# Optimization experiments

Hardware: AMD Instinct MI355X
Metric: run time of the kernel (lower is better)

## Reference

```python
import jax, jax.numpy as jnp
import numpy as np

HALF_LOG_2PI = 0.9189385332046727  # 0.5*log(2*pi)


def _sum_layer(prod, logits):
    # prod: [B, R, KK] child log-probs; logits: [R, KK, K] unnormalized sum weights
    W = jax.nn.softmax(logits, axis=1)            # normalized mixture weights
    m = jnp.max(prod, axis=-1, keepdims=True)     # stable logsumexp via einsum
    e = jnp.exp(prod - m)                         # [B, R, KK]
    s = jnp.einsum('brc,rck->brk', e, W)          # [B, R, K]
    return jnp.log(s) + m


def setup_inputs() -> dict:
    key = jax.random.key(0)
    ks = jax.random.split(key, 12)
    B, F, K = 8192, 256, 8
    inp = {
        'x': jax.random.normal(ks[0], (B, F), dtype=jnp.float32),
        'mu': jax.random.normal(ks[1], (F, K), dtype=jnp.float32),
        'log_sigma': jax.random.uniform(ks[2], (F, K), dtype=jnp.float32),
    }
    R = F // 2
    for i in range(8):
        inp['w%d' % i] = jax.random.normal(ks[3 + i], (R, K * K, K), dtype=jnp.float32)
        R //= 2
    inp['root_w'] = jax.random.normal(ks[11], (K,), dtype=jnp.float32)
    return inp


def reference(x, mu, log_sigma, w0, w1, w2, w3, w4, w5, w6, w7, root_w):
    # Gaussian leaf log-probs: [B, F, K]
    z = (x[:, :, None] - mu) * jnp.exp(-log_sigma)
    h = -0.5 * z * z - log_sigma - HALF_LOG_2PI
    # Alternating product (pair adjacent regions) / sum (mix KK -> K) layers
    for w in (w0, w1, w2, w3, w4, w5, w6, w7):
        B, R, K = h.shape
        prod = (h[:, 0::2, :, None] + h[:, 1::2, None, :]).reshape(B, R // 2, K * K)
        h = _sum_layer(prod, w)
    # Root sum node over the K dists of the single remaining region -> [B]
    lp = h[:, 0, :] + jax.nn.log_softmax(root_w)
    return jax.scipy.special.logsumexp(lp, axis=-1)
```

## Files before the change

kernel.cpp:

```cpp
#include <hip/hip_runtime.h>
#include <math.h>

#define NTH 256

static constexpr float HLP = 0.9189385332046727f;

typedef __attribute__((ext_vector_type(2))) _Float16 half2v;
typedef __attribute__((ext_vector_type(2))) __fp16   fp16x2;

static constexpr int WTTd = 61440;
static constexpr int AOF2 = 65280;
static constexpr int BOF2 = 67328;
static constexpr int ROF2 = 69376;
static constexpr int L1NF = 69632;
static constexpr int L1MF = L1NF + 2097152;
static constexpr int L3NF = L1MF + 524288;
static constexpr int L3MF = L3NF + 524288;
static constexpr size_t WS_NEED_B = (size_t)(L3MF + 131072) * 4;

__device__ __forceinline__ half2v pkrtz(float a, float b) {
  return __builtin_bit_cast(half2v, __builtin_amdgcn_cvt_pkrtz(a, b));
}
__device__ __forceinline__ half2v u2h(unsigned u) {
  return __builtin_bit_cast(half2v, u);
}
__device__ __forceinline__ unsigned h2u(half2v h) {
  return __builtin_bit_cast(unsigned, h);
}
__device__ __forceinline__ float dd(half2v a, half2v b, float c) {
#if __has_builtin(__builtin_amdgcn_fdot2)
  return __builtin_amdgcn_fdot2(__builtin_bit_cast(fp16x2, a),
                                __builtin_bit_cast(fp16x2, b), c, false);
#else
  return fmaf((float)a[0], (float)b[0], fmaf((float)a[1], (float)b[1], c));
#endif
}
__device__ __forceinline__ float max8(const float* s) {
  float m = s[0];
  #pragma unroll
  for (int k = 1; k < 8; ++k) m = fmaxf(m, s[k]);
  return m;
}

__device__ __forceinline__ void leaf_ii(float xv, const float* mu8, const float* A8,
                                        const float* B8, half2v* ii, float* M) {
  float h[8];
  float m = -3.0e38f;
  #pragma unroll
  for (int k = 0; k < 8; ++k) {
    const float z = (xv - mu8[k]) * A8[k];
    h[k] = fmaf(-0.5f * z, z, B8[k]);
    m = fmaxf(m, h[k]);
  }
  #pragma unroll
  for (int k = 0; k < 8; ++k) {
    const float n = __expf(h[k] - m);
    ii[k] = pkrtz(n, n);
  }
  *M = m;
}
__device__ __forceinline__ void leaf_pk(float xv, const float* mu8, const float* A8,
                                        const float* B8, half2v* pk, float* M) {
  float h[8];
  float m = -3.0e38f;
  #pragma unroll
  for (int k = 0; k < 8; ++k) {
    const float z = (xv - mu8[k]) * A8[k];
    h[k] = fmaf(-0.5f * z, z, B8[k]);
    m = fmaxf(m, h[k]);
  }
  #pragma unroll
  for (int p = 0; p < 4; ++p) {
    const float n0 = __expf(h[2 * p] - m);
    const float n1 = __expf(h[2 * p + 1] - m);
    pk[p] = pkrtz(n0, n1);
  }
  *M = m;
}

template<int G, bool OUT_II>
__device__ __forceinline__ void combine_d2(const uint4* __restrict__ WL,
                                           const half2v (&na)[G][8],
                                           const half2v (&nb)[G][4],
                                           half2v (&oii)[G][8],
                                           half2v (&opk)[G][4],
                                           float (&M)[G]) {
  float s[G][8];
  #pragma unroll
  for (int g = 0; g < G; ++g)
    #pragma unroll
    for (int k = 0; k < 8; ++k) s[g][k] = 0.f;

  #pragma unroll
  for (int i = 0; i < 8; ++i) {
    half2v e[G][4];
    #pragma unroll
    for (int g = 0; g < G; ++g) {
      e[g][0] = na[g][i] * nb[g][0];
      e[g][1] = na[g][i] * nb[g][1];
      e[g][2] = na[g][i] * nb[g][2];
      e[g][3] = na[g][i] * nb[g][3];
    }
    #pragma unroll
    for (int k = 0; k < 8; ++k) {
      const uint4 w = WL[i * 8 + k];
      #pragma unroll
      for (int g = 0; g < G; ++g) {
        float acc = s[g][k];
        acc = dd(e[g][0], u2h(w.x), acc);
        acc = dd(e[g][1], u2h(w.y), acc);
        acc = dd(e[g][2], u2h(w.z), acc);
        acc = dd(e[g][3], u2h(w.w), acc);
        s[g][k] = acc;
      }
    }
  }
  #pragma unroll
  for (int g = 0; g < G; ++g) {
    const float smax = max8(s[g]);
    const float inv = 1.0f / smax;
    if constexpr (OUT_II) {
      #pragma unroll
      for (int p = 0; p < 8; ++p) {
        const float n = s[g][p] * inv;
        oii[g][p] = pkrtz(n, n);
      }
    } else {
      #pragma unroll
      for (int p = 0; p < 4; ++p)
        opk[g][p] = pkrtz(s[g][2 * p] * inv, s[g][2 * p + 1] * inv);
    }
    M[g] += __logf(smax);
  }
}

__global__ __launch_bounds__(256) void spn_prep4(
    const float* __restrict__ ls,
    const float* __restrict__ w0, const float* __restrict__ w1,
    const float* __restrict__ w2, const float* __restrict__ w3,
    const float* __restrict__ w4, const float* __restrict__ w5,
    const float* __restrict__ w6, const float* __restrict__ w7,
    const float* __restrict__ root_w,
    float* __restrict__ ws)
{
  const int job = blockIdx.x * blockDim.x + threadIdx.x;
  unsigned* wdw = reinterpret_cast<unsigned*>(ws);
  if (job < 1920) {
    const int ridx = job >> 3, k = job & 7;
    const float* src;
    if (ridx < 128)      src = w0 + ridx * 512 + k;
    else if (ridx < 192) src = w1 + (ridx - 128) * 512 + k;
    else if (ridx < 224) src = w2 + (ridx - 192) * 512 + k;
    else                 src = w3 + (ridx - 224) * 512 + k;
    float v[64];
    float m = -3.0e38f;
    #pragma unroll
    for (int c = 0; c < 64; ++c) { v[c] = src[c * 8]; m = fmaxf(m, v[c]); }
    float t = 0.f;
    #pragma unroll
    for (int c = 0; c < 64; ++c) { v[c] = __expf(v[c] - m); t += v[c]; }
    const float inv = 1.0f / t;
    #pragma unroll
    for (int i = 0; i < 8; ++i)
      #pragma unroll
      for (int jp = 0; jp < 4; ++jp)
        wdw[ridx * 256 + (i * 8 + k) * 4 + jp] =
            h2u(pkrtz(v[i * 8 + 2 * jp] * inv, v[i * 8 + 2 * jp + 1] * inv));
  } else if (job < 2040) {
    const int j = job - 1920;
    const int reg = j >> 3, k = j & 7;
    const float* src;
    if (reg < 8)       src = w4 + reg * 512 + k;
    else if (reg < 12) src = w5 + (reg - 8) * 512 + k;
    else if (reg < 14) src = w6 + (reg - 12) * 512 + k;
    else               src = w7 + k;
    float v[64];
    float m = -3.0e38f;
    #pragma unroll
    for (int c = 0; c < 64; ++c) { v[c] = src[c * 8]; m = fmaxf(m, v[c]); }
    float t = 0.f;
    #pragma unroll
    for (int c = 0; c < 64; ++c) { v[c] = __expf(v[c] - m); t += v[c]; }
    const float inv = 1.0f / t;
    #pragma unroll
    for (int i = 0; i < 8; ++i)
      #pragma unroll
      for (int jp = 0; jp < 4; ++jp)
        wdw[WTTd + reg * 256 + k * 32 + (((i ^ k) & 7) << 2) + jp] =
            h2u(pkrtz(v[i * 8 + 2 * jp] * inv, v[i * 8 + 2 * jp + 1] * inv));
  } else if (job < 2040 + 2048) {
    const int i = job - 2040;
    const float l = ls[i];
    ws[AOF2 + i] = __expf(-l);
    ws[BOF2 + i] = -l - HLP;
  } else if (job == 2040 + 2048) {
    float m = -3.0e38f;
    for (int k = 0; k < 8; ++k) m = fmaxf(m, root_w[k]);
    float e[8]; float t = 0.f;
    for (int k = 0; k < 8; ++k) { e[k] = __expf(root_w[k] - m); t += e[k]; }
    const float inv = 1.0f / t;
    for (int k = 0; k < 8; ++k) ws[ROF2 + k] = e[k] * inv;
  }
}

__global__ __launch_bounds__(NTH, 4) void spn_L01d(
    const float* __restrict__ x,
    const float* __restrict__ mu,
    float* __restrict__ ws)
{
  __shared__ uint4 wsh4[192];
  __shared__ float lsh[96];
  const int tid = threadIdx.x;
  const int r1 = blockIdx.x >> 4;
  const int chunk = blockIdx.x & 15;
  const uint4* wg = reinterpret_cast<const uint4*>(ws);

  if (tid < 192) {
    const int reg = tid >> 6;
    const int rbase = (reg < 2) ? (2 * r1 + reg) : (128 + r1);
    wsh4[tid] = wg[rbase * 64 + (tid & 63)];
  }
  if (tid < 96) {
    const int f8 = r1 * 32;
    lsh[tid] = (tid < 32) ? mu[f8 + tid]
             : (tid < 64) ? ws[AOF2 + f8 + (tid - 32)]
                          : ws[BOF2 + f8 + (tid - 64)];
  }
  __syncthreads();

  const int b0 = chunk * 512 + tid;
  const float4 xv0 = *reinterpret_cast<const float4*>(x + (size_t)b0 * 256 + 4 * r1);
  const float4 xv1 = *reinterpret_cast<const float4*>(x + (size_t)(b0 + 256) * 256 + 4 * r1);

  half2v ii[2][8], pk[2][4];
  half2v cAii[2][8], cBpk[2][4];
  half2v dmy_ii[2][8], dmy_pk[2][4];
  float MA[2], MB[2];
  float Ma, Mb;

  leaf_ii(xv0.x, lsh + 0, lsh + 32, lsh + 64, ii[0], &Ma);
  leaf_pk(xv0.y, lsh + 8, lsh + 40, lsh + 72, pk[0], &Mb);
  MA[0] = Ma + Mb;
  leaf_ii(xv1.x, lsh + 0, lsh + 32, lsh + 64, ii[1], &Ma);
  leaf_pk(xv1.y, lsh + 8, lsh + 40, lsh + 72, pk[1], &Mb);
  MA[1] = Ma + Mb;
  combine_d2<2, true>(wsh4, ii, pk, cAii, dmy_pk, MA);

  leaf_ii(xv0.z, lsh + 16, lsh + 48, lsh + 80, ii[0], &Ma);
  leaf_pk(xv0.w, lsh + 24, lsh + 56, lsh + 88, pk[0], &Mb);
  MB[0] = Ma + Mb;
  leaf_ii(xv1.z, lsh + 16, lsh + 48, lsh + 80, ii[1], &Ma);
  leaf_pk(xv1.w, lsh + 24, lsh + 56, lsh + 88, pk[1], &Mb);
  MB[1] = Ma + Mb;
  combine_d2<2, false>(wsh4 + 64, ii, pk, dmy_ii, cBpk, MB);

  float M[2] = {MA[0] + MB[0], MA[1] + MB[1]};
  half2v n[2][4];
  combine_d2<2, false>(wsh4 + 128, cAii, cBpk, dmy_ii, n, M);

  uint4* outn = reinterpret_cast<uint4*>(ws + L1NF);
  outn[r1 * 8192 + b0]       = uint4{h2u(n[0][0]), h2u(n[0][1]), h2u(n[0][2]), h2u(n[0][3])};
  outn[r1 * 8192 + b0 + 256] = uint4{h2u(n[1][0]), h2u(n[1][1]), h2u(n[1][2]), h2u(n[1][3])};
  ws[L1MF + r1 * 8192 + b0]       = M[0];
  ws[L1MF + r1 * 8192 + b0 + 256] = M[1];
}

__device__ __forceinline__ void mk_ii(uint4 p, half2v* ii) {
  const half2v a0 = u2h(p.x), a1 = u2h(p.y), a2 = u2h(p.z), a3 = u2h(p.w);
  ii[0] = __builtin_shufflevector(a0, a0, 0, 0);
  ii[1] = __builtin_shufflevector(a0, a0, 1, 1);
  ii[2] = __builtin_shufflevector(a1, a1, 0, 0);
  ii[3] = __builtin_shufflevector(a1, a1, 1, 1);
  ii[4] = __builtin_shufflevector(a2, a2, 0, 0);
  ii[5] = __builtin_shufflevector(a2, a2, 1, 1);
  ii[6] = __builtin_shufflevector(a3, a3, 0, 0);
  ii[7] = __builtin_shufflevector(a3, a3, 1, 1);
}

__global__ __launch_bounds__(NTH, 4) void spn_L23d(float* __restrict__ ws)
{
  __shared__ uint4 wsh4[192];
  const int tid = threadIdx.x;
  const int r3 = blockIdx.x >> 5;
  const int chunk = blockIdx.x & 31;
  const uint4* wg = reinterpret_cast<const uint4*>(ws);

  if (tid < 192) {
    const int reg = tid >> 6;
    const int rbase = (reg < 2) ? (192 + 2 * r3 + reg) : (224 + r3);
    wsh4[tid] = wg[rbase * 64 + (tid & 63)];
  }
  __syncthreads();

  const int b = chunk * 256 + tid;
  const uint4* n4 = reinterpret_cast<const uint4*>(ws + L1NF);
  const uint4 p0 = n4[(4 * r3 + 0) * 8192 + b];
  const uint4 p1 = n4[(4 * r3 + 1) * 8192 + b];
  const uint4 p2 = n4[(4 * r3 + 2) * 8192 + b];
  const uint4 p3 = n4[(4 * r3 + 3) * 8192 + b];
  const float M0 = ws[L1MF + (4 * r3 + 0) * 8192 + b];
  const float M1 = ws[L1MF + (4 * r3 + 1) * 8192 + b];
  const float M2 = ws[L1MF + (4 * r3 + 2) * 8192 + b];
  const float M3 = ws[L1MF + (4 * r3 + 3) * 8192 + b];

  half2v ii[1][8], pk[1][4];
  half2v cAii[1][8], cBpk[1][4];
  half2v dmy_ii[1][8], dmy_pk[1][4];

  mk_ii(p0, ii[0]);
  pk[0][0] = u2h(p1.x); pk[0][1] = u2h(p1.y); pk[0][2] = u2h(p1.z); pk[0][3] = u2h(p1.w);
  float MA[1] = {M0 + M1};
  combine_d2<1, true>(wsh4, ii, pk, cAii, dmy_pk, MA);

  mk_ii(p2, ii[0]);
  pk[0][0] = u2h(p3.x); pk[0][1] = u2h(p3.y); pk[0][2] = u2h(p3.z); pk[0][3] = u2h(p3.w);
  float MB[1] = {M2 + M3};
  combine_d2<1, false>(wsh4 + 64, ii, pk, dmy_ii, cBpk, MB);

  float M[1] = {MA[0] + MB[0]};
  half2v n[1][4];
  combine_d2<1, false>(wsh4 + 128, cAii, cBpk, dmy_ii, n, M);

  reinterpret_cast<uint4*>(ws + L3NF)[r3 * 8192 + b] =
      uint4{h2u(n[0][0]), h2u(n[0][1]), h2u(n[0][2]), h2u(n[0][3])};
  ws[L3MF + r3 * 8192 + b] = M[0];
}

__device__ __forceinline__ float macTd(const uint4* __restrict__ Wr, int myk,
                                       const float* na, const half2v* nbpk) {
  float s = 0.f;
  #pragma unroll
  for (int i = 0; i < 8; ++i) {
    const uint4 w = Wr[myk * 8 + ((i ^ myk) & 7)];
    float T = dd(nbpk[0], u2h(w.x), 0.f);
    T = dd(nbpk[1], u2h(w.y), T);
    T = dd(nbpk[2], u2h(w.z), T);
    T = dd(nbpk[3], u2h(w.w), T);
    s = fmaf(na[i], T, s);
  }
  return s;
}

__global__ __launch_bounds__(NTH) void spn_taild(float* __restrict__ ws,
                                                 float* __restrict__ out)
{
  __shared__ uint4 wsh4[960];
  __shared__ float ssh[8];
  const int tid = threadIdx.x;
  const uint4* wg = reinterpret_cast<const uint4*>(ws);
  #pragma unroll
  for (int i = 0; i < 4; ++i) {
    const int idx = tid + i * 256;
    if (idx < 960) wsh4[idx] = wg[WTTd / 4 + idx];
  }
  if (tid < 8) ssh[tid] = ws[ROF2 + tid];
  __syncthreads();

  const int lane = tid & 63, wid = tid >> 6;
  const int myk = lane & 7, bsub = lane >> 3, gbase = lane & 56;
  const int b = blockIdx.x * 32 + wid * 8 + bsub;

  const uint4* n4 = reinterpret_cast<const uint4*>(ws + L3NF);

  float n4v[8], M4[8];
  #pragma unroll
  for (int r = 0; r < 8; ++r) {
    const uint4 pa = n4[(2 * r + 0) * 8192 + b];
    const uint4 pb = n4[(2 * r + 1) * 8192 + b];
    const float Ma = ws[L3MF + (2 * r + 0) * 8192 + b];
    const float Mb = ws[L3MF + (2 * r + 1) * 8192 + b];
    float na[8];
    const half2v a0 = u2h(pa.x), a1 = u2h(pa.y), a2 = u2h(pa.z), a3 = u2h(pa.w);
    na[0] = (float)a0[0]; na[1] = (float)a0[1];
    na[2] = (float)a1[0]; na[3] = (float)a1[1];
    na[4] = (float)a2[0]; na[5] = (float)a2[1];
    na[6] = (float)a3[0]; na[7] = (float)a3[1];
    half2v nbpk[4] = {u2h(pb.x), u2h(pb.y), u2h(pb.z), u2h(pb.w)};
    float s = macTd(wsh4 + r * 64, myk, na, nbpk);
    float m = s;
    m = fmaxf(m, __shfl_xor(m, 1)); m = fmaxf(m, __shfl_xor(m, 2)); m = fmaxf(m, __shfl_xor(m, 4));
    n4v[r] = s / m;
    M4[r] = Ma + Mb + __logf(m);
  }

  float n5v[4], M5[4];
  #pragma unroll
  for (int r = 0; r < 4; ++r) {
    float na[8]; half2v nbpk[4];
    #pragma unroll
    for (int i = 0; i < 8; ++i) na[i] = __shfl(n4v[2 * r], gbase + i, 64);
    #pragma unroll
    for (int p = 0; p < 4; ++p)
      nbpk[p] = pkrtz(__shfl(n4v[2 * r + 1], gbase + 2 * p, 64),
                      __shfl(n4v[2 * r + 1], gbase + 2 * p + 1, 64));
    float s = macTd(wsh4 + (8 + r) * 64, myk, na, nbpk);
    float m = s;
    m = fmaxf(m, __shfl_xor(m, 1)); m = fmaxf(m, __shfl_xor(m, 2)); m = fmaxf(m, __shfl_xor(m, 4));
    n5v[r] = s / m;
    M5[r] = M4[2 * r] + M4[2 * r + 1] + __logf(m);
  }

  float n6v[2], M6[2];
  #pragma unroll
  for (int r = 0; r < 2; ++r) {
    float na[8]; half2v nbpk[4];
    #pragma unroll
    for (int i = 0; i < 8; ++i) na[i] = __shfl(n5v[2 * r], gbase + i, 64);
    #pragma unroll
    for (int p = 0; p < 4; ++p)
      nbpk[p] = pkrtz(__shfl(n5v[2 * r + 1], gbase + 2 * p, 64),
                      __shfl(n5v[2 * r + 1], gbase + 2 * p + 1, 64));
    float s = macTd(wsh4 + (12 + r) * 64, myk, na, nbpk);
    float m = s;
    m = fmaxf(m, __shfl_xor(m, 1)); m = fmaxf(m, __shfl_xor(m, 2)); m = fmaxf(m, __shfl_xor(m, 4));
    n6v[r] = s / m;
    M6[r] = M5[2 * r] + M5[2 * r + 1] + __logf(m);
  }

  {
    float na[8]; half2v nbpk[4];
    #pragma unroll
    for (int i = 0; i < 8; ++i) na[i] = __shfl(n6v[0], gbase + i, 64);
    #pragma unroll
    for (int p = 0; p < 4; ++p)
      nbpk[p] = pkrtz(__shfl(n6v[1], gbase + 2 * p, 64),
                      __shfl(n6v[1], gbase + 2 * p + 1, 64));
    float s = macTd(wsh4 + 14 * 64, myk, na, nbpk);
    float m = s;
    m = fmaxf(m, __shfl_xor(m, 1)); m = fmaxf(m, __shfl_xor(m, 2)); m = fmaxf(m, __shfl_xor(m, 4));
    const float n7 = s / m;
    const float M7 = M6[0] + M6[1] + __logf(m);
    float prod = n7 * ssh[myk];
    prod += __shfl_xor(prod, 1); prod += __shfl_xor(prod, 2); prod += __shfl_xor(prod, 4);
    if (myk == 0) out[b] = M7 + __logf(prod);
  }
}

static constexpr int NW   = 130560;
static constexpr int AOFF = NW;
static constexpr int BOFF = NW + 2048;
static constexpr int ROFF = NW + 4096;

__device__ __forceinline__ void leaf_eval(float xv, const float* mu8, const float* A8,
                                          const float* B8, float* n, float* M) {
  float h[8];
  float m = -3.0e38f;
  #pragma unroll
  for (int k = 0; k < 8; ++k) {
    const float z = (xv - mu8[k]) * A8[k];
    h[k] = fmaf(-0.5f * z, z, B8[k]);
    m = fmaxf(m, h[k]);
  }
  #pragma unroll
  for (int k = 0; k < 8; ++k) n[k] = __expf(h[k] - m);
  *M = m;
}

__global__ __launch_bounds__(256) void spn_prep(
    const float* __restrict__ ls,
    const float* __restrict__ w0, const float* __restrict__ w1,
    const float* __restrict__ w2, const float* __restrict__ w3,
    const float* __restrict__ w4, const float* __restrict__ w5,
    const float* __restrict__ w6, const float* __restrict__ w7,
    const float* __restrict__ root_w,
    float* __restrict__ ws)
{
  const int job = blockIdx.x * blockDim.x + threadIdx.x;
  if (job < 2040) {
    const float* wl[8] = {w0, w1, w2, w3, w4, w5, w6, w7};
    int j = job, l = 0, base = 0, R = 128;
    while (j >= R * 8) { j -= R * 8; base += R * 512; R >>= 1; ++l; }
    const int r = j >> 3, k = j & 7;
    const float* src = wl[l] + r * 512 + k;
    float v[64];
    float m = -3.0e38f;
    #pragma unroll
    for (int c = 0; c < 64; ++c) { v[c] = src[c * 8]; m = fmaxf(m, v[c]); }
    float ssum = 0.f;
    #pragma unroll
    for (int c = 0; c < 64; ++c) { v[c] = __expf(v[c] - m); ssum += v[c]; }
    const float inv = 1.0f / ssum;
    float* dst = ws + base + r * 512 + k;
    #pragma unroll
    for (int c = 0; c < 64; ++c) dst[c * 8] = v[c] * inv;
  } else if (job < 2040 + 2048) {
    const int i = job - 2040;
    const float l = ls[i];
    ws[AOFF + i] = __expf(-l);
    ws[BOFF + i] = -l - HLP;
  } else if (job == 2040 + 2048) {
    float m = -3.0e38f;
    for (int k = 0; k < 8; ++k) m = fmaxf(m, root_w[k]);
    float e[8]; float ssum = 0.f;
    for (int k = 0; k < 8; ++k) { e[k] = __expf(root_w[k] - m); ssum += e[k]; }
    const float inv = 1.0f / ssum;
    for (int k = 0; k < 8; ++k) ws[ROFF + k] = e[k] * inv;
  }
}

__device__ __forceinline__ void mac64(const float* __restrict__ Wr,
                                      const float* na, const float* nb,
                                      float* s) {
  #pragma unroll
  for (int k = 0; k < 8; ++k) s[k] = 0.f;
  #pragma unroll
  for (int i = 0; i < 8; ++i) {
    const float ai = na[i];
    #pragma unroll
    for (int j = 0; j < 8; ++j) {
      const float e = ai * nb[j];
      const float4 wA = *reinterpret_cast<const float4*>(Wr + (i * 8 + j) * 8);
      const float4 wB = *reinterpret_cast<const float4*>(Wr + (i * 8 + j) * 8 + 4);
      s[0] = fmaf(e, wA.x, s[0]); s[1] = fmaf(e, wA.y, s[1]);
      s[2] = fmaf(e, wA.z, s[2]); s[3] = fmaf(e, wA.w, s[3]);
      s[4] = fmaf(e, wB.x, s[4]); s[5] = fmaf(e, wB.y, s[5]);
      s[6] = fmaf(e, wB.z, s[6]); s[7] = fmaf(e, wB.w, s[7]);
    }
  }
}

#define TB 8
static constexpr int PLA = 128 * 9 + 5;
static constexpr int PLB = 64 * 9 + 5;
static constexpr int NAO = 0;
static constexpr int NBO = TB * PLA;
static constexpr int MAO = NBO + TB * PLB;
static constexpr int MBO = MAO + TB * 128;
static constexpr int SMEM_F = MBO + TB * 64;

__global__ __launch_bounds__(NTH, 2) void spn_main_fb(
    const float* __restrict__ x,
    const float* __restrict__ mu,
    const float* __restrict__ ws,
    float* __restrict__ out)
{
  const float* leafA = ws + AOFF;
  const float* leafB = ws + BOFF;
  const float* srw   = ws + ROFF;

  __shared__ float smem[SMEM_F];

  const int tid = threadIdx.x;
  const int bB = blockIdx.x * TB;

  {
    const float* W0 = ws;
    for (int it = tid; it < TB * 128; it += NTH) {
      const int bb = it & (TB - 1), r = it >> 3;
      float na[8], nb[8], Ma, Mb;
      const int f0 = 2 * r;
      const float xv0 = x[(bB + bb) * 256 + f0];
      const float xv1 = x[(bB + bb) * 256 + f0 + 1];
      leaf_eval(xv0, mu + f0 * 8, leafA + f0 * 8, leafB + f0 * 8, na, &Ma);
      leaf_eval(xv1, mu + f0 * 8 + 8, leafA + f0 * 8 + 8, leafB + f0 * 8 + 8, nb, &Mb);
      float s[8];
      mac64(W0 + r * 512, na, nb, s);
      const float smax = max8(s);
      const float inv = 1.0f / smax;
      const int ob = NAO + bb * PLA + r * 9;
      #pragma unroll
      for (int k = 0; k < 8; ++k) smem[ob + k] = s[k] * inv;
      smem[MAO + bb * 128 + r] = Ma + Mb + __logf(smax);
    }
  }
  __syncthreads();

  int pinO = NAO, poutO = NBO;
  int MinO = MAO, MoutO = MBO;
  int PLIN = PLA, PLOUT = PLB;
  int Rin = 128;
  const float* Wl = ws + 128 * 512;
  for (int l = 1; l < 7; ++l) {
    const int Rout = Rin >> 1;
    for (int it = tid; it < TB * Rout; it += NTH) {
      const int bb = it & (TB - 1), r = it >> 3;
      float na[8], nb[8];
      const int ia = pinO + bb * PLIN + (2 * r) * 9;
      #pragma unroll
      for (int i = 0; i < 8; ++i) { na[i] = smem[ia + i]; nb[i] = smem[ia + 9 + i]; }
      float s[8];
      mac64(Wl + r * 512, na, nb, s);
      const float smax = max8(s);
      const float inv = 1.0f / smax;
      const int ob = poutO + bb * PLOUT + r * 9;
      #pragma unroll
      for (int k = 0; k < 8; ++k) smem[ob + k] = s[k] * inv;
      smem[MoutO + bb * Rout + r] =
          smem[MinO + bb * Rin + 2 * r] + smem[MinO + bb * Rin + 2 * r + 1] + __logf(smax);
    }
    __syncthreads();
    int t;
    t = pinO; pinO = poutO; poutO = t;
    t = MinO; MinO = MoutO; MoutO = t;
    t = PLIN; PLIN = PLOUT; PLOUT = t;
    Rin = Rout;
    Wl += Rout * 512;
  }

  for (int it = tid; it < TB; it += NTH) {
    const int bb = it;
    float na[8], nb[8];
    const int ia = pinO + bb * PLIN;
    #pragma unroll
    for (int i = 0; i < 8; ++i) { na[i] = smem[ia + i]; nb[i] = smem[ia + 9 + i]; }
    float s[8];
    mac64(Wl, na, nb, s);
    float acc = 0.f;
    #pragma unroll
    for (int k = 0; k < 8; ++k) acc = fmaf(s[k], srw[k], acc);
    out[bB + bb] = smem[MinO + bb * 2] + smem[MinO + bb * 2 + 1] + __logf(acc);
  }
}

extern "C" void kernel_launch(void* const* d_in, const int* in_sizes, int n_in,
                              void* d_out, int out_size, void* d_ws, size_t ws_size,
                              hipStream_t stream) {
  (void)in_sizes; (void)n_in; (void)out_size;
  const float* x      = (const float*)d_in[0];
  const float* mu     = (const float*)d_in[1];
  const float* ls     = (const float*)d_in[2];
  const float* w0     = (const float*)d_in[3];
  const float* w1     = (const float*)d_in[4];
  const float* w2     = (const float*)d_in[5];
  const float* w3     = (const float*)d_in[6];
  const float* w4     = (const float*)d_in[7];
  const float* w5     = (const float*)d_in[8];
  const float* w6     = (const float*)d_in[9];
  const float* w7     = (const float*)d_in[10];
  const float* root_w = (const float*)d_in[11];
  float* ws  = (float*)d_ws;
  float* out = (float*)d_out;

  if (ws_size >= WS_NEED_B) {
    spn_prep4<<<16, 256, 0, stream>>>(ls, w0, w1, w2, w3, w4, w5, w6, w7, root_w, ws);
    spn_L01d<<<1024, NTH, 0, stream>>>(x, mu, ws);
    spn_L23d<<<512, NTH, 0, stream>>>(ws);
    spn_taild<<<256, NTH, 0, stream>>>(ws, out);
  } else {
    spn_prep<<<16, 256, 0, stream>>>(ls, w0, w1, w2, w3, w4, w5, w6, w7, root_w, ws);
    spn_main_fb<<<8192 / TB, NTH, 0, stream>>>(x, mu, ws, out);
  }
}
```

Measured before the change: 57.25 us.

## Parallelize weight prep per region and batch more samples per thread

The prep kernel now uses one block per weight region. Each block stages 512 logits in shared memory with coalesced loads, and eight threads then compute the softmax, instead of 16 blocks whose threads read with stride. The L01 and L23 kernels each process twice as many samples per thread and launch half as many blocks, which amortizes the shared-memory weight loads and raises ILP. The cost is higher register pressure (L01 launch bounds lowered to 3 waves) and fewer blocks to hide latency.

```diff
diff --git a/kernel.cpp b/kernel.cpp
--- a/kernel.cpp
+++ b/kernel.cpp
@@ -134,7 +134,7 @@
   }
 }
 
-__global__ __launch_bounds__(256) void spn_prep4(
+__global__ __launch_bounds__(256) void spn_prep5(
     const float* __restrict__ ls,
     const float* __restrict__ w0, const float* __restrict__ w1,
     const float* __restrict__ w2, const float* __restrict__ w3,
@@ -143,67 +143,78 @@
     const float* __restrict__ root_w,
     float* __restrict__ ws)
 {
-  const int job = blockIdx.x * blockDim.x + threadIdx.x;
+  const int blk = blockIdx.x;
+  const int tid = threadIdx.x;
   unsigned* wdw = reinterpret_cast<unsigned*>(ws);
-  if (job < 1920) {
-    const int ridx = job >> 3, k = job & 7;
-    const float* src;
-    if (ridx < 128)      src = w0 + ridx * 512 + k;
-    else if (ridx < 192) src = w1 + (ridx - 128) * 512 + k;
-    else if (ridx < 224) src = w2 + (ridx - 192) * 512 + k;
-    else                 src = w3 + (ridx - 224) * 512 + k;
+
+  if (blk == 255) {
+    #pragma unroll
+    for (int i = 0; i < 8; ++i) {
+      const int idx = tid + i * 256;
+      const float l = ls[idx];
+      ws[AOF2 + idx] = __expf(-l);
+      ws[BOF2 + idx] = -l - HLP;
+    }
+    if (tid == 0) {
+      float m = -3.0e38f;
+      for (int k = 0; k < 8; ++k) m = fmaxf(m, root_w[k]);
+      float e[8]; float t = 0.f;
+      for (int k = 0; k < 8; ++k) { e[k] = __expf(root_w[k] - m); t += e[k]; }
+      const float inv = 1.0f / t;
+      for (int k = 0; k < 8; ++k) ws[ROF2 + k] = e[k] * inv;
+    }
+    return;
+  }
+
+  __shared__ float lsw[512];
+  const float* src;
+  bool transposed = false;
+  int reg = 0;
+  if (blk < 128)       src = w0 + blk * 512;
+  else if (blk < 192)  src = w1 + (blk - 128) * 512;
+  else if (blk < 224)  src = w2 + (blk - 192) * 512;
+  else if (blk < 240)  src = w3 + (blk - 224) * 512;
+  else {
+    transposed = true;
+    reg = blk - 240;
+    if (reg < 8)       src = w4 + reg * 512;
+    else if (reg < 12) src = w5 + (reg - 8) * 512;
+    else if (reg < 14) src = w6 + (reg - 12) * 512;
+    else               src = w7;
+  }
+  lsw[tid]       = src[tid];
+  lsw[tid + 256] = src[tid + 256];
+  __syncthreads();
+
+  if (tid < 8) {
+    const int k = tid;
     float v[64];
     float m = -3.0e38f;
     #pragma unroll
-    for (int c = 0; c < 64; ++c) { v[c] = src[c * 8]; m = fmaxf(m, v[c]); }
+    for (int c = 0; c < 64; ++c) { v[c] = lsw[c * 8 + k]; m = fmaxf(m, v[c]); }
     float t = 0.f;
     #pragma unroll
     for (int c = 0; c < 64; ++c) { v[c] = __expf(v[c] - m); t += v[c]; }
     const float inv = 1.0f / t;
-    #pragma unroll
-    for (int i = 0; i < 8; ++i)
-      #pragma unroll
-      for (int jp = 0; jp < 4; ++jp)
-        wdw[ridx * 256 + (i * 8 + k) * 4 + jp] =
-            h2u(pkrtz(v[i * 8 + 2 * jp] * inv, v[i * 8 + 2 * jp + 1] * inv));
-  } else if (job < 2040) {
-    const int j = job - 1920;
-    const int reg = j >> 3, k = j & 7;
-    const float* src;
-    if (reg < 8)       src = w4 + reg * 512 + k;
-    else if (reg < 12) src = w5 + (reg - 8) * 512 + k;
-    else if (reg < 14) src = w6 + (reg - 12) * 512 + k;
-    else               src = w7 + k;
-    float v[64];
-    float m = -3.0e38f;
-    #pragma unroll
-    for (int c = 0; c < 64; ++c) { v[c] = src[c * 8]; m = fmaxf(m, v[c]); }
-    float t = 0.f;
-    #pragma unroll
-    for (int c = 0; c < 64; ++c) { v[c] = __expf(v[c] - m); t += v[c]; }
-    const float inv = 1.0f / t;
-    #pragma unroll
-    for (int i = 0; i < 8; ++i)
-      #pragma unroll
-      for (int jp = 0; jp < 4; ++jp)
-        wdw[WTTd + reg * 256 + k * 32 + (((i ^ k) & 7) << 2) + jp] =
-            h2u(pkrtz(v[i * 8 + 2 * jp] * inv, v[i * 8 + 2 * jp + 1] * inv));
-  } else if (job < 2040 + 2048) {
-    const int i = job - 2040;
-    const float l = ls[i];
-    ws[AOF2 + i] = __expf(-l);
-    ws[BOF2 + i] = -l - HLP;
-  } else if (job == 2040 + 2048) {
-    float m = -3.0e38f;
-    for (int k = 0; k < 8; ++k) m = fmaxf(m, root_w[k]);
-    float e[8]; float t = 0.f;
-    for (int k = 0; k < 8; ++k) { e[k] = __expf(root_w[k] - m); t += e[k]; }
-    const float inv = 1.0f / t;
-    for (int k = 0; k < 8; ++k) ws[ROF2 + k] = e[k] * inv;
-  }
-}
-
-__global__ __launch_bounds__(NTH, 4) void spn_L01d(
+    if (!transposed) {
+      #pragma unroll
+      for (int i = 0; i < 8; ++i)
+        #pragma unroll
+        for (int jp = 0; jp < 4; ++jp)
+          wdw[blk * 256 + (i * 8 + k) * 4 + jp] =
+              h2u(pkrtz(v[i * 8 + 2 * jp] * inv, v[i * 8 + 2 * jp + 1] * inv));
+    } else {
+      #pragma unroll
+      for (int i = 0; i < 8; ++i)
+        #pragma unroll
+        for (int jp = 0; jp < 4; ++jp)
+          wdw[WTTd + reg * 256 + k * 32 + (((i ^ k) & 7) << 2) + jp] =
+              h2u(pkrtz(v[i * 8 + 2 * jp] * inv, v[i * 8 + 2 * jp + 1] * inv));
+    }
+  }
+}
+
+__global__ __launch_bounds__(NTH, 3) void spn_L01e(
     const float* __restrict__ x,
     const float* __restrict__ mu,
     float* __restrict__ ws)
@@ -211,8 +222,8 @@
   __shared__ uint4 wsh4[192];
   __shared__ float lsh[96];
   const int tid = threadIdx.x;
-  const int r1 = blockIdx.x >> 4;
-  const int chunk = blockIdx.x & 15;
+  const int r1 = blockIdx.x >> 3;
+  const int chunk = blockIdx.x & 7;
   const uint4* wg = reinterpret_cast<const uint4*>(ws);
 
   if (tid < 192) {
@@ -228,41 +239,47 @@
   }
   __syncthreads();
 
-  const int b0 = chunk * 512 + tid;
-  const float4 xv0 = *reinterpret_cast<const float4*>(x + (size_t)b0 * 256 + 4 * r1);
-  const float4 xv1 = *reinterpret_cast<const float4*>(x + (size_t)(b0 + 256) * 256 + 4 * r1);
-
-  half2v ii[2][8], pk[2][4];
-  half2v cAii[2][8], cBpk[2][4];
-  half2v dmy_ii[2][8], dmy_pk[2][4];
-  float MA[2], MB[2];
+  const int b0 = chunk * 1024 + tid;
+  float4 xv[4];
+  #pragma unroll
+  for (int g = 0; g < 4; ++g)
+    xv[g] = *reinterpret_cast<const float4*>(x + (size_t)(b0 + 256 * g) * 256 + 4 * r1);
+
+  half2v ii[4][8], pk[4][4];
+  half2v cAii[4][8], cBpk[4][4];
+  half2v dmy_ii[4][8], dmy_pk[4][4];
+  float MA[4], MB[4];
   float Ma, Mb;
 
-  leaf_ii(xv0.x, lsh + 0, lsh + 32, lsh + 64, ii[0], &Ma);
-  leaf_pk(xv0.y, lsh + 8, lsh + 40, lsh + 72, pk[0], &Mb);
-  MA[0] = Ma + Mb;
-  leaf_ii(xv1.x, lsh + 0, lsh + 32, lsh + 64, ii[1], &Ma);
-  leaf_pk(xv1.y, lsh + 8, lsh + 40, lsh + 72, pk[1], &Mb);
-  MA[1] = Ma + Mb;
-  combine_d2<2, true>(wsh4, ii, pk, cAii, dmy_pk, MA);
-
-  leaf_ii(xv0.z, lsh + 16, lsh + 48, lsh + 80, ii[0], &Ma);
-  leaf_pk(xv0.w, lsh + 24, lsh + 56, lsh + 88, pk[0], &Mb);
-  MB[0] = Ma + Mb;
-  leaf_ii(xv1.z, lsh + 16, lsh + 48, lsh + 80, ii[1], &Ma);
-  leaf_pk(xv1.w, lsh + 24, lsh + 56, lsh + 88, pk[1], &Mb);
-  MB[1] = Ma + Mb;
-  combine_d2<2, false>(wsh4 + 64, ii, pk, dmy_ii, cBpk, MB);
-
-  float M[2] = {MA[0] + MB[0], MA[1] + MB[1]};
-  half2v n[2][4];
-  combine_d2<2, false>(wsh4 + 128, cAii, cBpk, dmy_ii, n, M);
+  #pragma unroll
+  for (int g = 0; g < 4; ++g) {
+    leaf_ii(xv[g].x, lsh + 0, lsh + 32, lsh + 64, ii[g], &Ma);
+    leaf_pk(xv[g].y, lsh + 8, lsh + 40, lsh + 72, pk[g], &Mb);
+    MA[g] = Ma + Mb;
+  }
+  combine_d2<4, true>(wsh4, ii, pk, cAii, dmy_pk, MA);
+
+  #pragma unroll
+  for (int g = 0; g < 4; ++g) {
+    leaf_ii(xv[g].z, lsh + 16, lsh + 48, lsh + 80, ii[g], &Ma);
+    leaf_pk(xv[g].w, lsh + 24, lsh + 56, lsh + 88, pk[g], &Mb);
+    MB[g] = Ma + Mb;
+  }
+  combine_d2<4, false>(wsh4 + 64, ii, pk, dmy_ii, cBpk, MB);
+
+  float M[4];
+  #pragma unroll
+  for (int g = 0; g < 4; ++g) M[g] = MA[g] + MB[g];
+  half2v n[4][4];
+  combine_d2<4, false>(wsh4 + 128, cAii, cBpk, dmy_ii, n, M);
 
   uint4* outn = reinterpret_cast<uint4*>(ws + L1NF);
-  outn[r1 * 8192 + b0]       = uint4{h2u(n[0][0]), h2u(n[0][1]), h2u(n[0][2]), h2u(n[0][3])};
-  outn[r1 * 8192 + b0 + 256] = uint4{h2u(n[1][0]), h2u(n[1][1]), h2u(n[1][2]), h2u(n[1][3])};
-  ws[L1MF + r1 * 8192 + b0]       = M[0];
-  ws[L1MF + r1 * 8192 + b0 + 256] = M[1];
+  #pragma unroll
+  for (int g = 0; g < 4; ++g) {
+    outn[r1 * 8192 + b0 + 256 * g] =
+        uint4{h2u(n[g][0]), h2u(n[g][1]), h2u(n[g][2]), h2u(n[g][3])};
+    ws[L1MF + r1 * 8192 + b0 + 256 * g] = M[g];
+  }
 }
 
 __device__ __forceinline__ void mk_ii(uint4 p, half2v* ii) {
@@ -277,12 +294,12 @@
   ii[7] = __builtin_shufflevector(a3, a3, 1, 1);
 }
 
-__global__ __launch_bounds__(NTH, 4) void spn_L23d(float* __restrict__ ws)
+__global__ __launch_bounds__(NTH, 4) void spn_L23e(float* __restrict__ ws)
 {
   __shared__ uint4 wsh4[192];
   const int tid = threadIdx.x;
-  const int r3 = blockIdx.x >> 5;
-  const int chunk = blockIdx.x & 31;
+  const int r3 = blockIdx.x >> 4;
+  const int chunk = blockIdx.x & 15;
   const uint4* wg = reinterpret_cast<const uint4*>(ws);
 
   if (tid < 192) {
@@ -292,38 +309,46 @@
   }
   __syncthreads();
 
-  const int b = chunk * 256 + tid;
+  const int b0 = chunk * 512 + tid;
   const uint4* n4 = reinterpret_cast<const uint4*>(ws + L1NF);
-  const uint4 p0 = n4[(4 * r3 + 0) * 8192 + b];
-  const uint4 p1 = n4[(4 * r3 + 1) * 8192 + b];
-  const uint4 p2 = n4[(4 * r3 + 2) * 8192 + b];
-  const uint4 p3 = n4[(4 * r3 + 3) * 8192 + b];
-  const float M0 = ws[L1MF + (4 * r3 + 0) * 8192 + b];
-  const float M1 = ws[L1MF + (4 * r3 + 1) * 8192 + b];
-  const float M2 = ws[L1MF + (4 * r3 + 2) * 8192 + b];
-  const float M3 = ws[L1MF + (4 * r3 + 3) * 8192 + b];
-
-  half2v ii[1][8], pk[1][4];
-  half2v cAii[1][8], cBpk[1][4];
-  half2v dmy_ii[1][8], dmy_pk[1][4];
-
-  mk_ii(p0, ii[0]);
-  pk[0][0] = u2h(p1.x); pk[0][1] = u2h(p1.y); pk[0][2] = u2h(p1.z); pk[0][3] = u2h(p1.w);
-  float MA[1] = {M0 + M1};
-  combine_d2<1, true>(wsh4, ii, pk, cAii, dmy_pk, MA);
-
-  mk_ii(p2, ii[0]);
-  pk[0][0] = u2h(p3.x); pk[0][1] = u2h(p3.y); pk[0][2] = u2h(p3.z); pk[0][3] = u2h(p3.w);
-  float MB[1] = {M2 + M3};
-  combine_d2<1, false>(wsh4 + 64, ii, pk, dmy_ii, cBpk, MB);
-
-  float M[1] = {MA[0] + MB[0]};
-  half2v n[1][4];
-  combine_d2<1, false>(wsh4 + 128, cAii, cBpk, dmy_ii, n, M);
-
-  reinterpret_cast<uint4*>(ws + L3NF)[r3 * 8192 + b] =
-      uint4{h2u(n[0][0]), h2u(n[0][1]), h2u(n[0][2]), h2u(n[0][3])};
-  ws[L3MF + r3 * 8192 + b] = M[0];
+
+  half2v ii[2][8], pk[2][4];
+  half2v cAii[2][8], cBpk[2][4];
+  half2v dmy_ii[2][8], dmy_pk[2][4];
+  float MA[2], MB[2];
+
+  #pragma unroll
+  for (int g = 0; g < 2; ++g) {
+    const int b = b0 + 256 * g;
+    const uint4 p0 = n4[(4 * r3 + 0) * 8192 + b];
+    const uint4 p1 = n4[(4 * r3 + 1) * 8192 + b];
+    mk_ii(p0, ii[g]);
+    pk[g][0] = u2h(p1.x); pk[g][1] = u2h(p1.y); pk[g][2] = u2h(p1.z); pk[g][3] = u2h(p1.w);
+    MA[g] = ws[L1MF + (4 * r3 + 0) * 8192 + b] + ws[L1MF + (4 * r3 + 1) * 8192 + b];
+  }
+  combine_d2<2, true>(wsh4, ii, pk, cAii, dmy_pk, MA);
+
+  #pragma unroll
+  for (int g = 0; g < 2; ++g) {
+    const int b = b0 + 256 * g;
+    const uint4 p2 = n4[(4 * r3 + 2) * 8192 + b];
+    const uint4 p3 = n4[(4 * r3 + 3) * 8192 + b];
+    mk_ii(p2, ii[g]);
+    pk[g][0] = u2h(p3.x); pk[g][1] = u2h(p3.y); pk[g][2] = u2h(p3.z); pk[g][3] = u2h(p3.w);
+    MB[g] = ws[L1MF + (4 * r3 + 2) * 8192 + b] + ws[L1MF + (4 * r3 + 3) * 8192 + b];
+  }
+  combine_d2<2, false>(wsh4 + 64, ii, pk, dmy_ii, cBpk, MB);
+
+  float M[2] = {MA[0] + MB[0], MA[1] + MB[1]};
+  half2v n[2][4];
+  combine_d2<2, false>(wsh4 + 128, cAii, cBpk, dmy_ii, n, M);
+
+  #pragma unroll
+  for (int g = 0; g < 2; ++g) {
+    reinterpret_cast<uint4*>(ws + L3NF)[r3 * 8192 + b0 + 256 * g] =
+        uint4{h2u(n[g][0]), h2u(n[g][1]), h2u(n[g][2]), h2u(n[g][3])};
+    ws[L3MF + r3 * 8192 + b0 + 256 * g] = M[g];
+  }
 }
 
 __device__ __forceinline__ float macTd(const uint4* __restrict__ Wr, int myk,
@@ -632,9 +657,9 @@
   float* out = (float*)d_out;
 
   if (ws_size >= WS_NEED_B) {
-    spn_prep4<<<16, 256, 0, stream>>>(ls, w0, w1, w2, w3, w4, w5, w6, w7, root_w, ws);
-    spn_L01d<<<1024, NTH, 0, stream>>>(x, mu, ws);
-    spn_L23d<<<512, NTH, 0, stream>>>(ws);
+    spn_prep5<<<256, 256, 0, stream>>>(ls, w0, w1, w2, w3, w4, w5, w6, w7, root_w, ws);
+    spn_L01e<<<512, NTH, 0, stream>>>(x, mu, ws);
+    spn_L23e<<<256, NTH, 0, stream>>>(ws);
     spn_taild<<<256, NTH, 0, stream>>>(ws, out);
   } else {
     spn_prep<<<16, 256, 0, stream>>>(ls, w0, w1, w2, w3, w4, w5, w6, w7, root_w, ws);
```

New measurement: 59.41 us. 3.8% more time.

## Fold weight softmax prep into each layer kernel, drop separate prep launch

Applied to the files above, without the earlier changes.

Removes the standalone prep kernel and has each layer kernel stage its raw sum-weight slices in shared memory and compute the softmax-normalized fp16 weights locally, along with leaf sigma terms and root softmax. This eliminates one kernel launch and its serial dependency, at the cost of redundant softmax work per block (each of the 16/32 chunk blocks and all 256 tail blocks recompute the same weights) and extra shared memory and a second barrier per block.

```diff
diff --git a/kernel.cpp b/kernel.cpp
--- a/kernel.cpp
+++ b/kernel.cpp
@@ -8,15 +8,10 @@
 typedef __attribute__((ext_vector_type(2))) _Float16 half2v;
 typedef __attribute__((ext_vector_type(2))) __fp16   fp16x2;
 
-static constexpr int WTTd = 61440;
-static constexpr int AOF2 = 65280;
-static constexpr int BOF2 = 67328;
-static constexpr int ROF2 = 69376;
-static constexpr int L1NF = 69632;
-static constexpr int L1MF = L1NF + 2097152;
-static constexpr int L3NF = L1MF + 524288;
-static constexpr int L3MF = L3NF + 524288;
-static constexpr size_t WS_NEED_B = (size_t)(L3MF + 131072) * 4;
+static constexpr int L1MF = 2097152;
+static constexpr int L3NF = 2621440;
+static constexpr int L3MF = 3145728;
+static constexpr size_t WS_NEED_B = (size_t)3276800 * 4;
 
 __device__ __forceinline__ half2v pkrtz(float a, float b) {
   return __builtin_bit_cast(half2v, __builtin_amdgcn_cvt_pkrtz(a, b));
@@ -134,98 +129,57 @@
   }
 }
 
-__global__ __launch_bounds__(256) void spn_prep4(
+__device__ __forceinline__ void prep_col_std(const float* stage, unsigned* wdwL,
+                                             int r, int k) {
+  float v[64];
+  float m = -3.0e38f;
+  #pragma unroll
+  for (int c = 0; c < 64; ++c) { v[c] = stage[r * 512 + c * 8 + k]; m = fmaxf(m, v[c]); }
+  float t = 0.f;
+  #pragma unroll
+  for (int c = 0; c < 64; ++c) { v[c] = __expf(v[c] - m); t += v[c]; }
+  const float inv = 1.0f / t;
+  #pragma unroll
+  for (int i = 0; i < 8; ++i)
+    #pragma unroll
+    for (int jp = 0; jp < 4; ++jp)
+      wdwL[r * 256 + (i * 8 + k) * 4 + jp] =
+          h2u(pkrtz(v[i * 8 + 2 * jp] * inv, v[i * 8 + 2 * jp + 1] * inv));
+}
+
+__global__ __launch_bounds__(NTH, 4) void spn_a(
+    const float* __restrict__ x,
+    const float* __restrict__ mu,
     const float* __restrict__ ls,
-    const float* __restrict__ w0, const float* __restrict__ w1,
-    const float* __restrict__ w2, const float* __restrict__ w3,
-    const float* __restrict__ w4, const float* __restrict__ w5,
-    const float* __restrict__ w6, const float* __restrict__ w7,
-    const float* __restrict__ root_w,
+    const float* __restrict__ w0,
+    const float* __restrict__ w1,
     float* __restrict__ ws)
 {
-  const int job = blockIdx.x * blockDim.x + threadIdx.x;
-  unsigned* wdw = reinterpret_cast<unsigned*>(ws);
-  if (job < 1920) {
-    const int ridx = job >> 3, k = job & 7;
-    const float* src;
-    if (ridx < 128)      src = w0 + ridx * 512 + k;
-    else if (ridx < 192) src = w1 + (ridx - 128) * 512 + k;
-    else if (ridx < 224) src = w2 + (ridx - 192) * 512 + k;
-    else                 src = w3 + (ridx - 224) * 512 + k;
-    float v[64];
-    float m = -3.0e38f;
-    #pragma unroll
-    for (int c = 0; c < 64; ++c) { v[c] = src[c * 8]; m = fmaxf(m, v[c]); }
-    float t = 0.f;
-    #pragma unroll
-    for (int c = 0; c < 64; ++c) { v[c] = __expf(v[c] - m); t += v[c]; }
-    const float inv = 1.0f / t;
-    #pragma unroll
-    for (int i = 0; i < 8; ++i)
-      #pragma unroll
-      for (int jp = 0; jp < 4; ++jp)
-        wdw[ridx * 256 + (i * 8 + k) * 4 + jp] =
-            h2u(pkrtz(v[i * 8 + 2 * jp] * inv, v[i * 8 + 2 * jp + 1] * inv));
-  } else if (job < 2040) {
-    const int j = job - 1920;
-    const int reg = j >> 3, k = j & 7;
-    const float* src;
-    if (reg < 8)       src = w4 + reg * 512 + k;
-    else if (reg < 12) src = w5 + (reg - 8) * 512 + k;
-    else if (reg < 14) src = w6 + (reg - 12) * 512 + k;
-    else               src = w7 + k;
-    float v[64];
-    float m = -3.0e38f;
-    #pragma unroll
-    for (int c = 0; c < 64; ++c) { v[c] = src[c * 8]; m = fmaxf(m, v[c]); }
-    float t = 0.f;
-    #pragma unroll
-    for (int c = 0; c < 64; ++c) { v[c] = __expf(v[c] - m); t += v[c]; }
-    const float inv = 1.0f / t;
-    #pragma unroll
-    for (int i = 0; i < 8; ++i)
-      #pragma unroll
-      for (int jp = 0; jp < 4; ++jp)
-        wdw[WTTd + reg * 256 + k * 32 + (((i ^ k) & 7) << 2) + jp] =
-            h2u(pkrtz(v[i * 8 + 2 * jp] * inv, v[i * 8 + 2 * jp + 1] * inv));
-  } else if (job < 2040 + 2048) {
-    const int i = job - 2040;
-    const float l = ls[i];
-    ws[AOF2 + i] = __expf(-l);
-    ws[BOF2 + i] = -l - HLP;
-  } else if (job == 2040 + 2048) {
-    float m = -3.0e38f;
-    for (int k = 0; k < 8; ++k) m = fmaxf(m, root_w[k]);
-    float e[8]; float t = 0.f;
-    for (int k = 0; k < 8; ++k) { e[k] = __expf(root_w[k] - m); t += e[k]; }
-    const float inv = 1.0f / t;
-    for (int k = 0; k < 8; ++k) ws[ROF2 + k] = e[k] * inv;
-  }
-}
-
-__global__ __launch_bounds__(NTH, 4) void spn_L01d(
-    const float* __restrict__ x,
-    const float* __restrict__ mu,
-    float* __restrict__ ws)
-{
+  __shared__ float stage[1536];
   __shared__ uint4 wsh4[192];
   __shared__ float lsh[96];
   const int tid = threadIdx.x;
   const int r1 = blockIdx.x >> 4;
   const int chunk = blockIdx.x & 15;
-  const uint4* wg = reinterpret_cast<const uint4*>(ws);
-
-  if (tid < 192) {
-    const int reg = tid >> 6;
-    const int rbase = (reg < 2) ? (2 * r1 + reg) : (128 + r1);
-    wsh4[tid] = wg[rbase * 64 + (tid & 63)];
+
+  #pragma unroll
+  for (int i = 0; i < 6; ++i) {
+    const int idx = tid + 256 * i;
+    const int reg = idx >> 9, off = idx & 511;
+    const float* src = (reg == 0) ? (w0 + (2 * r1) * 512)
+                     : (reg == 1) ? (w0 + (2 * r1 + 1) * 512)
+                                  : (w1 + r1 * 512);
+    stage[idx] = src[off];
   }
   if (tid < 96) {
     const int f8 = r1 * 32;
-    lsh[tid] = (tid < 32) ? mu[f8 + tid]
-             : (tid < 64) ? ws[AOF2 + f8 + (tid - 32)]
-                          : ws[BOF2 + f8 + (tid - 64)];
-  }
+    if (tid < 32)      lsh[tid] = mu[f8 + tid];
+    else if (tid < 64) lsh[tid] = __expf(-ls[f8 + (tid - 32)]);
+    else               lsh[tid] = -ls[f8 + (tid - 64)] - HLP;
+  }
+  __syncthreads();
+
+  if (tid < 24) prep_col_std(stage, reinterpret_cast<unsigned*>(wsh4), tid >> 3, tid & 7);
   __syncthreads();
 
   const int b0 = chunk * 512 + tid;
@@ -258,7 +212,7 @@
   half2v n[2][4];
   combine_d2<2, false>(wsh4 + 128, cAii, cBpk, dmy_ii, n, M);
 
-  uint4* outn = reinterpret_cast<uint4*>(ws + L1NF);
+  uint4* outn = reinterpret_cast<uint4*>(ws);
   outn[r1 * 8192 + b0]       = uint4{h2u(n[0][0]), h2u(n[0][1]), h2u(n[0][2]), h2u(n[0][3])};
   outn[r1 * 8192 + b0 + 256] = uint4{h2u(n[1][0]), h2u(n[1][1]), h2u(n[1][2]), h2u(n[1][3])};
   ws[L1MF + r1 * 8192 + b0]       = M[0];
@@ -277,23 +231,32 @@
   ii[7] = __builtin_shufflevector(a3, a3, 1, 1);
 }
 
-__global__ __launch_bounds__(NTH, 4) void spn_L23d(float* __restrict__ ws)
+__global__ __launch_bounds__(NTH, 4) void spn_b(
+    const float* __restrict__ w2,
+    const float* __restrict__ w3,
+    float* __restrict__ ws)
 {
+  __shared__ float stage[1536];
   __shared__ uint4 wsh4[192];
   const int tid = threadIdx.x;
   const int r3 = blockIdx.x >> 5;
   const int chunk = blockIdx.x & 31;
-  const uint4* wg = reinterpret_cast<const uint4*>(ws);
-
-  if (tid < 192) {
-    const int reg = tid >> 6;
-    const int rbase = (reg < 2) ? (192 + 2 * r3 + reg) : (224 + r3);
-    wsh4[tid] = wg[rbase * 64 + (tid & 63)];
+
+  #pragma unroll
+  for (int i = 0; i < 6; ++i) {
+    const int idx = tid + 256 * i;
+    const int reg = idx >> 9, off = idx & 511;
+    const float* src = (reg == 0) ? (w2 + (2 * r3) * 512)
+                     : (reg == 1) ? (w2 + (2 * r3 + 1) * 512)
+                                  : (w3 + r3 * 512);
+    stage[idx] = src[off];
   }
   __syncthreads();
+  if (tid < 24) prep_col_std(stage, reinterpret_cast<unsigned*>(wsh4), tid >> 3, tid & 7);
+  __syncthreads();
 
   const int b = chunk * 256 + tid;
-  const uint4* n4 = reinterpret_cast<const uint4*>(ws + L1NF);
+  const uint4* n4 = reinterpret_cast<const uint4*>(ws);
   const uint4 p0 = n4[(4 * r3 + 0) * 8192 + b];
   const uint4 p1 = n4[(4 * r3 + 1) * 8192 + b];
   const uint4 p2 = n4[(4 * r3 + 2) * 8192 + b];
@@ -341,19 +304,57 @@
   return s;
 }
 
-__global__ __launch_bounds__(NTH) void spn_taild(float* __restrict__ ws,
-                                                 float* __restrict__ out)
+__global__ __launch_bounds__(NTH) void spn_c(
+    const float* __restrict__ w4, const float* __restrict__ w5,
+    const float* __restrict__ w6, const float* __restrict__ w7,
+    const float* __restrict__ root_w,
+    float* __restrict__ ws,
+    float* __restrict__ out)
 {
+  __shared__ float stage[7680];
   __shared__ uint4 wsh4[960];
   __shared__ float ssh[8];
   const int tid = threadIdx.x;
-  const uint4* wg = reinterpret_cast<const uint4*>(ws);
-  #pragma unroll
-  for (int i = 0; i < 4; ++i) {
-    const int idx = tid + i * 256;
-    if (idx < 960) wsh4[idx] = wg[WTTd / 4 + idx];
-  }
-  if (tid < 8) ssh[tid] = ws[ROF2 + tid];
+
+  #pragma unroll
+  for (int i = 0; i < 30; ++i) {
+    const int idx = tid + 256 * i;
+    const int reg = idx >> 9, off = idx & 511;
+    const float* src;
+    if (reg < 8)       src = w4 + reg * 512;
+    else if (reg < 12) src = w5 + (reg - 8) * 512;
+    else if (reg < 14) src = w6 + (reg - 12) * 512;
+    else               src = w7;
+    stage[idx] = src[off];
+  }
+  if (tid == 255) {
+    float m = -3.0e38f;
+    for (int k = 0; k < 8; ++k) m = fmaxf(m, root_w[k]);
+    float e[8]; float t = 0.f;
+    for (int k = 0; k < 8; ++k) { e[k] = __expf(root_w[k] - m); t += e[k]; }
+    const float inv = 1.0f / t;
+    for (int k = 0; k < 8; ++k) ssh[k] = e[k] * inv;
+  }
+  __syncthreads();
+
+  if (tid < 120) {
+    const int reg = tid >> 3, k = tid & 7;
+    float v[64];
+    float m = -3.0e38f;
+    #pragma unroll
+    for (int c = 0; c < 64; ++c) { v[c] = stage[reg * 512 + c * 8 + k]; m = fmaxf(m, v[c]); }
+    float t = 0.f;
+    #pragma unroll
+    for (int c = 0; c < 64; ++c) { v[c] = __expf(v[c] - m); t += v[c]; }
+    const float inv = 1.0f / t;
+    unsigned* wdwL = reinterpret_cast<unsigned*>(wsh4);
+    #pragma unroll
+    for (int i = 0; i < 8; ++i)
+      #pragma unroll
+      for (int jp = 0; jp < 4; ++jp)
+        wdwL[reg * 256 + k * 32 + (((i ^ k) & 7) << 2) + jp] =
+            h2u(pkrtz(v[i * 8 + 2 * jp] * inv, v[i * 8 + 2 * jp + 1] * inv));
+  }
   __syncthreads();
 
   const int lane = tid & 63, wid = tid >> 6;
@@ -632,10 +633,9 @@
   float* out = (float*)d_out;
 
   if (ws_size >= WS_NEED_B) {
-    spn_prep4<<<16, 256, 0, stream>>>(ls, w0, w1, w2, w3, w4, w5, w6, w7, root_w, ws);
-    spn_L01d<<<1024, NTH, 0, stream>>>(x, mu, ws);
-    spn_L23d<<<512, NTH, 0, stream>>>(ws);
-    spn_taild<<<256, NTH, 0, stream>>>(ws, out);
+    spn_a<<<1024, NTH, 0, stream>>>(x, mu, ls, w0, w1, ws);
+    spn_b<<<512, NTH, 0, stream>>>(w2, w3, ws);
+    spn_c<<<256, NTH, 0, stream>>>(w4, w5, w6, w7, root_w, ws, out);
   } else {
     spn_prep<<<16, 256, 0, stream>>>(ls, w0, w1, w2, w3, w4, w5, w6, w7, root_w, ws);
     spn_main_fb<<<8192 / TB, NTH, 0, stream>>>(x, mu, ws, out);
```

After: 51.75 us. 9.6% less time.
